# Kernel optimization log

Measured on AMD Instinct MI355X. Metric: run time of the kernel, lower is better.

Reference implementation:

```python
import jax, jax.numpy as jnp
import numpy as np

N_NODES = 50000
N_EDGES = 800000
IN_C, HID_C, OUT_C = 128, 128, 64
BN_EPS = 1e-5


def _normalized_adj(edge_index, N):
    # Mirrors remove_self_loops + add_self_loops + symmetric GCN normalization.
    src, dst = edge_index[0], edge_index[1]
    mask = (src != dst).astype(jnp.float32)  # drop original self loops
    # degree of dst over (masked edges + added self loops)
    deg = jax.ops.segment_sum(mask, dst, num_segments=N) + 1.0
    dinv = jnp.where(deg > 0, deg ** -0.5, 0.0)
    w = mask * dinv[src] * dinv[dst]          # weights for original edges
    w_self = dinv * dinv                      # weights for added self loops
    return src, dst, w, w_self


def _spmm(src, dst, w, w_self, x):
    # torch.sparse.mm(adj, x): out[i] = sum_{e: src[e]=i} w[e] * x[dst[e]] + w_self[i]*x[i]
    agg = jax.ops.segment_sum(w[:, None] * x[dst], src, num_segments=x.shape[0])
    return agg + w_self[:, None] * x


def setup_inputs() -> dict:
    key = jax.random.key(0)
    ks = jax.random.split(key, 4)
    x = jax.random.normal(ks[0], (N_NODES, IN_C), dtype=jnp.float32)
    edge_index = jax.random.randint(ks[1], (2, N_EDGES), 0, N_NODES, dtype=jnp.int64)
    # glorot init for GCN linear weights
    s1 = np.sqrt(6.0 / (IN_C + HID_C)).astype(np.float32)
    s2 = np.sqrt(6.0 / (HID_C + OUT_C)).astype(np.float32)
    W1 = jax.random.uniform(ks[2], (IN_C, HID_C), jnp.float32, -s1, s1)
    W2 = jax.random.uniform(ks[3], (HID_C, OUT_C), jnp.float32, -s2, s2)
    return {
        "x": x,
        "edge_index": edge_index,
        "W1": W1,
        "b1": jnp.zeros((HID_C,), jnp.float32),
        "gamma": jnp.ones((HID_C,), jnp.float32),
        "beta": jnp.zeros((HID_C,), jnp.float32),
        "W2": W2,
        "b2": jnp.zeros((OUT_C,), jnp.float32),
    }


def reference(x, edge_index, W1, b1, gamma, beta, W2, b2):
    N = x.shape[0]
    src, dst, w, w_self = _normalized_adj(edge_index, N)
    # layer 1: linear -> SpMM -> BN (batch stats) -> ReLU (dropout: eval)
    h = x @ W1 + b1
    h = _spmm(src, dst, w, w_self, h)
    mean = h.mean(axis=0)
    var = jnp.mean((h - mean) ** 2, axis=0)
    h = (h - mean) * jax.lax.rsqrt(var + BN_EPS) * gamma + beta
    h = jax.nn.relu(h)
    # layer 2: linear -> SpMM
    h = h @ W2 + b2
    h = _spmm(src, dst, w, w_self, h)
    return h
```

## Files before the change

### kernel.cpp

```cpp
#include <hip/hip_runtime.h>

#define N_NODES 50000
#define N_EDGES 800000
#define BN_EPS 1e-5f
#define NPAD 50176
#define SCAN_BLOCKS 98

#define S_SLICES 64
#define R_RANGES 7
#define BINS 8192
#define NP7 (R_RANGES * BINS)
#define ES (N_EDGES / S_SLICES)

#define XS_STRIDE 68

typedef unsigned int uint;
typedef unsigned short ushort;
typedef float floatx4 __attribute__((ext_vector_type(4)));
typedef short bf16x8 __attribute__((ext_vector_type(8)));

__device__ __forceinline__ float bfl(uint u) { return __uint_as_float(u << 16); }
__device__ __forceinline__ float bfh(uint u) { return __uint_as_float(u & 0xffff0000u); }
__device__ __forceinline__ uint pack_bf2(float a, float b) {
    uint ua = __float_as_uint(a), ub = __float_as_uint(b);
    ua += 0x7fffu + ((ua >> 16) & 1u);
    ub += 0x7fffu + ((ub >> 16) & 1u);
    return (ua >> 16) | (ub & 0xffff0000u);
}
__device__ __forceinline__ ushort bf1(float x) {
    uint u = __float_as_uint(x);
    u += 0x7fffu + ((u >> 16) & 1u);
    return (ushort)(u >> 16);
}
__device__ __forceinline__ void acc8(float* a, uint4 h, float w) {
    a[0] += w * bfl(h.x); a[1] += w * bfh(h.x);
    a[2] += w * bfl(h.y); a[3] += w * bfh(h.y);
    a[4] += w * bfl(h.z); a[5] += w * bfh(h.z);
    a[6] += w * bfl(h.w); a[7] += w * bfh(h.w);
}

__global__ __launch_bounds__(256) void prep_w_kernel(const float* __restrict__ W1,
                                                     const float* __restrict__ W2,
                                                     uint* __restrict__ W1t,
                                                     uint* __restrict__ W2t) {
    int t = blockIdx.x * 256 + threadIdx.x;
    if (t < 8192) {
        int n = t >> 6, kk = t & 63;
        W1t[t] = pack_bf2(W1[(2 * kk) * 128 + n], W1[(2 * kk + 1) * 128 + n]);
    } else if (t < 12288) {
        int u = t - 8192;
        int n = u >> 6, kk = u & 63;
        W2t[u] = pack_bf2(W2[(2 * kk) * 64 + n], W2[(2 * kk + 1) * 64 + n]);
    }
}

__global__ __launch_bounds__(256) void count_hist_kernel(const int* __restrict__ src,
                                                         const int* __restrict__ dst,
                                                         ushort* __restrict__ part_cnt,
                                                         ushort* __restrict__ part_deg) {
    __shared__ uint cnt_lds[BINS];
    __shared__ uint deg_lds[BINS];
    const int s = blockIdx.x / R_RANGES;
    const int r = blockIdx.x % R_RANGES;
    const int base = r * BINS;
    for (int j = threadIdx.x; j < BINS; j += 256) { cnt_lds[j] = 0u; deg_lds[j] = 0u; }
    __syncthreads();
    const int e0 = s * ES;
    for (int i = threadIdx.x; i < ES; i += 256) {
        int e = e0 + i;
        int ss = src[e], dd = dst[e];
        if (ss != dd) {
            int a = ss - base;
            if ((unsigned)a < (unsigned)BINS) atomicAdd(&cnt_lds[a], 1u);
            int b = dd - base;
            if ((unsigned)b < (unsigned)BINS) atomicAdd(&deg_lds[b], 1u);
        }
    }
    __syncthreads();
    uint* pc = (uint*)&part_cnt[s * NP7 + base];
    uint* pd = (uint*)&part_deg[s * NP7 + base];
    for (int j = threadIdx.x; j < BINS / 2; j += 256) {
        pc[j] = (cnt_lds[2 * j] & 0xffffu) | (cnt_lds[2 * j + 1] << 16);
        pd[j] = (deg_lds[2 * j] & 0xffffu) | (deg_lds[2 * j + 1] << 16);
    }
}

__global__ __launch_bounds__(256) void dinv_rowcnt_kernel(const ushort* __restrict__ part_deg,
                                                          const ushort* __restrict__ part_cnt,
                                                          float* __restrict__ dinv,
                                                          int* __restrict__ rowcnt) {
    int i = (blockIdx.x * 256 + threadIdx.x) * 2;
    uint dg0 = 0, dg1 = 0, rc0 = 0, rc1 = 0;
#pragma unroll 8
    for (int s = 0; s < S_SLICES; ++s) {
        uint vd = *(const uint*)&part_deg[s * NP7 + i];
        uint vc = *(const uint*)&part_cnt[s * NP7 + i];
        dg0 += vd & 0xffffu; dg1 += vd >> 16;
        rc0 += vc & 0xffffu; rc1 += vc >> 16;
    }
    *(int2*)&rowcnt[i] = make_int2((int)rc0, (int)rc1);
    if (i < N_NODES) dinv[i] = rsqrtf((float)dg0 + 1.0f);
    if (i + 1 < N_NODES) dinv[i + 1] = rsqrtf((float)dg1 + 1.0f);
}

__global__ __launch_bounds__(512) void scan1_kernel(const int* __restrict__ rowcnt,
                                                    int* __restrict__ rowptr,
                                                    int* __restrict__ psum) {
    __shared__ int buf[512];
    int t = threadIdx.x;
    int g = blockIdx.x * 512 + t;
    buf[t] = rowcnt[g];
    __syncthreads();
#pragma unroll
    for (int off = 1; off < 512; off <<= 1) {
        int x = (t >= off) ? buf[t - off] : 0;
        __syncthreads();
        buf[t] += x;
        __syncthreads();
    }
    rowptr[g] = buf[t];
    if (t == 511) psum[blockIdx.x] = buf[511];
}

__global__ void scan2_kernel(int* __restrict__ psum) {
    if (threadIdx.x == 0) {
        int acc = 0;
        for (int i = 0; i < SCAN_BLOCKS; ++i) {
            int v = psum[i];
            psum[i] = acc;
            acc += v;
        }
    }
}

__global__ __launch_bounds__(512) void scan3_kernel(const int* __restrict__ rowcnt,
                                                    int* __restrict__ rowptr,
                                                    const int* __restrict__ psum) {
    int t = threadIdx.x;
    int g = blockIdx.x * 512 + t;
    rowptr[g] = rowptr[g] - rowcnt[g] + psum[blockIdx.x];
}

__global__ __launch_bounds__(256) void cursor_init_kernel(const int* __restrict__ rowptr,
                                                          const ushort* __restrict__ part_cnt,
                                                          int* __restrict__ cursor) {
    int i = (blockIdx.x * 256 + threadIdx.x) * 2;
    int b0 = rowptr[i], b1 = rowptr[i + 1];
#pragma unroll 8
    for (int s = 0; s < S_SLICES; ++s) {
        *(int2*)&cursor[s * NP7 + i] = make_int2(b0, b1);
        uint vc = *(const uint*)&part_cnt[s * NP7 + i];
        b0 += (int)(vc & 0xffffu);
        b1 += (int)(vc >> 16);
    }
}

__global__ __launch_bounds__(256) void fill_lds_kernel(const int* __restrict__ src,
                                                       const int* __restrict__ dst,
                                                       const float* __restrict__ dinv,
                                                       const int* __restrict__ cursor,
                                                       int2* __restrict__ epair) {
    __shared__ int curs[BINS];
    const int s = blockIdx.x / R_RANGES;
    const int r = blockIdx.x % R_RANGES;
    const int base = r * BINS;
    const int* gc = &cursor[s * NP7 + base];
    for (int j = threadIdx.x; j < BINS; j += 256) curs[j] = gc[j];
    __syncthreads();
    const int e0 = s * ES;
    for (int i = threadIdx.x; i < ES; i += 256) {
        int e = e0 + i;
        int ss = src[e], dd = dst[e];
        int a = ss - base;
        if (ss != dd && (unsigned)a < (unsigned)BINS) {
            int pos = atomicAdd(&curs[a], 1);
            epair[pos] = make_int2(dd, __float_as_int(dinv[ss] * dinv[dd]));
        }
    }
}

__global__ __launch_bounds__(256) void gemm1_mfma_kernel(const float* __restrict__ X,
                                                         const uint* __restrict__ W1t,
                                                         const float* __restrict__ bias,
                                                         ushort* __restrict__ Hbf) {
    __shared__ uint lds[(64 + 128) * XS_STRIDE];
    uint* Xs = lds;
    uint* Ws = lds + 64 * XS_STRIDE;
    const int t = threadIdx.x;
    const int rowBase = blockIdx.x * 64;

    {
        int r = t >> 2, q = t & 3;
        int arow = rowBase + r;
        uint* xd = &Xs[r * XS_STRIDE + q * 16];
        if (arow < N_NODES) {
            const float4* xp = (const float4*)&X[arow * 128 + q * 32];
#pragma unroll
            for (int i = 0; i < 8; ++i) {
                float4 v = xp[i];
                xd[2 * i]     = pack_bf2(v.x, v.y);
                xd[2 * i + 1] = pack_bf2(v.z, v.w);
            }
        } else {
#pragma unroll
            for (int i = 0; i < 16; ++i) xd[i] = 0u;
        }
    }
    {
        int n = t >> 1, half = t & 1;
        const uint4* wp = (const uint4*)&W1t[n * 64 + half * 32];
        uint* wd = &Ws[n * XS_STRIDE + half * 32];
#pragma unroll
        for (int i = 0; i < 8; ++i) *(uint4*)&wd[i * 4] = wp[i];
    }
    __syncthreads();

    const int wv = t >> 6, lane = t & 63;
    const int lr = lane & 15;
    const int ko = (lane >> 4) * 4;
    const int m0 = wv * 16;
    floatx4 acc[8];
#pragma unroll
    for (int j = 0; j < 8; ++j) acc[j] = (floatx4){0.f, 0.f, 0.f, 0.f};

#pragma unroll
    for (int ks = 0; ks < 4; ++ks) {
        const int kb = ks * 16 + ko;
        bf16x8 a = *(bf16x8*)&Xs[(m0 + lr) * XS_STRIDE + kb];
#pragma unroll
        for (int j = 0; j < 8; ++j) {
            bf16x8 b = *(bf16x8*)&Ws[(j * 16 + lr) * XS_STRIDE + kb];
            acc[j] = __builtin_amdgcn_mfma_f32_16x16x32_bf16(a, b, acc[j], 0, 0, 0);
        }
    }
    const int rbase = rowBase + m0 + (lane >> 4) * 4;
#pragma unroll
    for (int j = 0; j < 8; ++j) {
        const int col = j * 16 + lr;
        const float bb = bias[col];
#pragma unroll
        for (int r = 0; r < 4; ++r) {
            int row = rbase + r;
            if (row < N_NODES) Hbf[row * 128 + col] = bf1(acc[j][r] + bb);
        }
    }
}

__global__ __launch_bounds__(256) void gemm2_mfma_kernel(const float* __restrict__ Hin,
                                                         const uint* __restrict__ W2t,
                                                         const float* __restrict__ bias,
                                                         const float* __restrict__ scale,
                                                         const float* __restrict__ shift,
                                                         ushort* __restrict__ Hbf) {
    __shared__ uint lds[(64 + 64) * XS_STRIDE];
    uint* Xs = lds;
    uint* Ws = lds + 64 * XS_STRIDE;
    const int t = threadIdx.x;
    const int rowBase = blockIdx.x * 64;

    {
        int r = t >> 2, q = t & 3;
        int arow = rowBase + r;
        uint* xd = &Xs[r * XS_STRIDE + q * 16];
        if (arow < N_NODES) {
            const float4* xp  = (const float4*)&Hin[arow * 128 + q * 32];
            const float4* sc4 = (const float4*)&scale[q * 32];
            const float4* sh4 = (const float4*)&shift[q * 32];
#pragma unroll
            for (int i = 0; i < 8; ++i) {
                float4 v = xp[i], sc = sc4[i], sh = sh4[i];
                float a0 = fmaxf(0.f, v.x * sc.x + sh.x);
                float a1 = fmaxf(0.f, v.y * sc.y + sh.y);
                float a2 = fmaxf(0.f, v.z * sc.z + sh.z);
                float a3 = fmaxf(0.f, v.w * sc.w + sh.w);
                xd[2 * i]     = pack_bf2(a0, a1);
                xd[2 * i + 1] = pack_bf2(a2, a3);
            }
        } else {
#pragma unroll
            for (int i = 0; i < 16; ++i) xd[i] = 0u;
        }
    }
    if (t < 128) {
        int n = t >> 1, half = t & 1;
        const uint4* wp = (const uint4*)&W2t[n * 64 + half * 32];
        uint* wd = &Ws[n * XS_STRIDE + half * 32];
#pragma unroll
        for (int i = 0; i < 8; ++i) *(uint4*)&wd[i * 4] = wp[i];
    }
    __syncthreads();

    const int wv = t >> 6, lane = t & 63;
    const int lr = lane & 15;
    const int ko = (lane >> 4) * 4;
    const int m0 = wv * 16;
    floatx4 acc[4];
#pragma unroll
    for (int j = 0; j < 4; ++j) acc[j] = (floatx4){0.f, 0.f, 0.f, 0.f};

#pragma unroll
    for (int ks = 0; ks < 4; ++ks) {
        const int kb = ks * 16 + ko;
        bf16x8 a = *(bf16x8*)&Xs[(m0 + lr) * XS_STRIDE + kb];
#pragma unroll
        for (int j = 0; j < 4; ++j) {
            bf16x8 b = *(bf16x8*)&Ws[(j * 16 + lr) * XS_STRIDE + kb];
            acc[j] = __builtin_amdgcn_mfma_f32_16x16x32_bf16(a, b, acc[j], 0, 0, 0);
        }
    }
    const int rbase = rowBase + m0 + (lane >> 4) * 4;
#pragma unroll
    for (int j = 0; j < 4; ++j) {
        const int col = j * 16 + lr;
        const float bb = bias[col];
#pragma unroll
        for (int r = 0; r < 4; ++r) {
            int row = rbase + r;
            if (row < N_NODES) Hbf[row * 64 + col] = bf1(acc[j][r] + bb);
        }
    }
}

template <int C>
__global__ __launch_bounds__(256) void spmm_bf16_kernel(const int* __restrict__ rowptr,
                                                        const int2* __restrict__ epair,
                                                        const float* __restrict__ dinv,
                                                        const uint* __restrict__ H,
                                                        float* __restrict__ out) {
    constexpr int LPR = C / 8;
    constexpr int RPB = 256 / LPR;
    constexpr int US  = C / 2;
    const int t = threadIdx.x;
    const int lane = t % LPR;
    const int row = blockIdx.x * RPB + t / LPR;
    if (row >= N_NODES) return;
    const int cu = lane * 4;
    const float di = dinv[row];

    float acc[8];
    {
        uint4 hv = *(const uint4*)&H[row * US + cu];
        float w = di * di;
        acc[0] = w * bfl(hv.x); acc[1] = w * bfh(hv.x);
        acc[2] = w * bfl(hv.y); acc[3] = w * bfh(hv.y);
        acc[4] = w * bfl(hv.z); acc[5] = w * bfh(hv.z);
        acc[6] = w * bfl(hv.w); acc[7] = w * bfh(hv.w);
    }
    const int e0 = rowptr[row], e1 = rowptr[row + 1];
    int e = e0;
    for (; e + 4 <= e1; e += 4) {
        int2 p0 = epair[e + 0], p1 = epair[e + 1], p2 = epair[e + 2], p3 = epair[e + 3];
        uint4 h0 = *(const uint4*)&H[p0.x * US + cu];
        uint4 h1 = *(const uint4*)&H[p1.x * US + cu];
        uint4 h2 = *(const uint4*)&H[p2.x * US + cu];
        uint4 h3 = *(const uint4*)&H[p3.x * US + cu];
        acc8(acc, h0, __int_as_float(p0.y));
        acc8(acc, h1, __int_as_float(p1.y));
        acc8(acc, h2, __int_as_float(p2.y));
        acc8(acc, h3, __int_as_float(p3.y));
    }
    for (; e < e1; ++e) {
        int2 p = epair[e];
        uint4 h = *(const uint4*)&H[p.x * US + cu];
        acc8(acc, h, __int_as_float(p.y));
    }
    float4 o0 = make_float4(acc[0], acc[1], acc[2], acc[3]);
    float4 o1 = make_float4(acc[4], acc[5], acc[6], acc[7]);
    *(float4*)&out[row * C + lane * 8] = o0;
    *(float4*)&out[row * C + lane * 8 + 4] = o1;
}

__global__ __launch_bounds__(256) void bn_stats_kernel(const float* __restrict__ H,
                                                       float* __restrict__ sum,
                                                       float* __restrict__ sumsq) {
    int c = threadIdx.x & 127;
    int half = threadIdx.x >> 7;
    float s = 0.f, q = 0.f;
    for (int r = blockIdx.x * 2 + half; r < N_NODES; r += 512) {
        float v = H[r * 128 + c];
        s += v;
        q += v * v;
    }
    __shared__ float ls[256], lq[256];
    ls[threadIdx.x] = s;
    lq[threadIdx.x] = q;
    __syncthreads();
    if (half == 0) {
        atomicAdd(&sum[c], ls[c] + ls[c + 128]);
        atomicAdd(&sumsq[c], lq[c] + lq[c + 128]);
    }
}

__global__ void bn_finalize_kernel(const float* __restrict__ sum,
                                   const float* __restrict__ sumsq,
                                   const float* __restrict__ gamma,
                                   const float* __restrict__ beta,
                                   float* __restrict__ scale,
                                   float* __restrict__ shift) {
    int c = threadIdx.x;
    if (c < 128) {
        float mean = sum[c] * (1.0f / N_NODES);
        float var = sumsq[c] * (1.0f / N_NODES) - mean * mean;
        float sc = gamma[c] * rsqrtf(var + BN_EPS);
        scale[c] = sc;
        shift[c] = beta[c] - mean * sc;
    }
}

extern "C" void kernel_launch(void* const* d_in, const int* in_sizes, int n_in,
                              void* d_out, int out_size, void* d_ws, size_t ws_size,
                              hipStream_t stream) {
    const float* x     = (const float*)d_in[0];
    const int*   ei    = (const int*)d_in[1];
    const float* W1    = (const float*)d_in[2];
    const float* b1    = (const float*)d_in[3];
    const float* gamma = (const float*)d_in[4];
    const float* beta  = (const float*)d_in[5];
    const float* W2    = (const float*)d_in[6];
    const float* b2    = (const float*)d_in[7];
    float* out = (float*)d_out;
    const int* src = ei;
    const int* dst = ei + N_EDGES;

    float* ws     = (float*)d_ws;
    float* dinv   = ws;
    float* stats  = ws + NPAD;
    int*   psum   = (int*)(ws + NPAD + 512);
    int*   rowcnt = psum + 128;
    int*   rowptr = rowcnt + NPAD;
    float* big    = (float*)(rowptr + NPAD);
    ushort* part_cnt = (ushort*)big;
    ushort* part_deg = part_cnt + S_SLICES * NP7;
    int*    cursor   = (int*)(part_deg + S_SLICES * NP7);
    ushort* h1bf  = (ushort*)big;
    float*  h1agg = big + 3200000;
    int2*   epair = (int2*)(big + 9600000);
    uint*   W1t   = (uint*)(big + 11200000);
    uint*   W2t   = W1t + 8192;
    ushort* h2bf  = h1bf;
    float* sum    = stats;
    float* sumsq  = stats + 128;
    float* scale  = stats + 256;
    float* shift  = stats + 384;

    hipMemsetAsync(stats, 0, 512 * sizeof(float), stream);

    prep_w_kernel<<<48, 256, 0, stream>>>(W1, W2, W1t, W2t);

    count_hist_kernel<<<S_SLICES * R_RANGES, 256, 0, stream>>>(src, dst, part_cnt, part_deg);
    dinv_rowcnt_kernel<<<NPAD / 512, 256, 0, stream>>>(part_deg, part_cnt, dinv, rowcnt);

    scan1_kernel<<<SCAN_BLOCKS, 512, 0, stream>>>(rowcnt, rowptr, psum);
    scan2_kernel<<<1, 64, 0, stream>>>(psum);
    scan3_kernel<<<SCAN_BLOCKS, 512, 0, stream>>>(rowcnt, rowptr, psum);
    cursor_init_kernel<<<NPAD / 512, 256, 0, stream>>>(rowptr, part_cnt, cursor);
    fill_lds_kernel<<<S_SLICES * R_RANGES, 256, 0, stream>>>(src, dst, dinv, cursor, epair);

    gemm1_mfma_kernel<<<(N_NODES + 63) / 64, 256, 0, stream>>>(x, W1t, b1, h1bf);

    spmm_bf16_kernel<128><<<(N_NODES + 15) / 16, 256, 0, stream>>>(rowptr, epair, dinv,
                                                                   (const uint*)h1bf, h1agg);

    bn_stats_kernel<<<256, 256, 0, stream>>>(h1agg, sum, sumsq);
    bn_finalize_kernel<<<1, 128, 0, stream>>>(sum, sumsq, gamma, beta, scale, shift);

    gemm2_mfma_kernel<<<(N_NODES + 63) / 64, 256, 0, stream>>>(h1agg, W2t, b2, scale, shift, h2bf);

    spmm_bf16_kernel<64><<<(N_NODES + 31) / 32, 256, 0, stream>>>(rowptr, epair, dinv,
                                                                  (const uint*)h2bf, out);
}
```

Measured before the change: 277.4 us.

## Store layer-1 SpMM output in bf16, degree-sort rows, pack 16-bit histograms, fuse scan

Several changes land together. The layer-1 SpMM now writes bf16 instead of fp32, which halves the traffic for bn_stats and gemm2, and bn_stats is rewritten to read packed bf16. Rows are permuted by degree bucket, built with a histogram, a scan and a scatter, so wavefronts in the SpMM kernels get similar loop lengths. The count histogram packs two 16-bit counters per LDS word, which allows 4 ranges of 16384 bins instead of 7 of 8192, and scan3 is folded into cursor_init. In exchange it adds three small kernels and bf16 rounding of pre-BN activations, and the permuted rows lose write locality.

```diff
diff --git a/kernel.cpp b/kernel.cpp
--- a/kernel.cpp
+++ b/kernel.cpp
@@ -7,9 +7,9 @@
 #define SCAN_BLOCKS 98
 
 #define S_SLICES 64
-#define R_RANGES 7
-#define BINS 8192
-#define NP7 (R_RANGES * BINS)
+#define R_RANGES 4
+#define BINS 16384
+#define NP4 (R_RANGES * BINS)
 #define ES (N_EDGES / S_SLICES)
 
 #define XS_STRIDE 68
@@ -58,12 +58,12 @@
                                                          const int* __restrict__ dst,
                                                          ushort* __restrict__ part_cnt,
                                                          ushort* __restrict__ part_deg) {
-    __shared__ uint cnt_lds[BINS];
-    __shared__ uint deg_lds[BINS];
+    __shared__ uint cnt_lds[BINS / 2];
+    __shared__ uint deg_lds[BINS / 2];
     const int s = blockIdx.x / R_RANGES;
     const int r = blockIdx.x % R_RANGES;
     const int base = r * BINS;
-    for (int j = threadIdx.x; j < BINS; j += 256) { cnt_lds[j] = 0u; deg_lds[j] = 0u; }
+    for (int j = threadIdx.x; j < BINS / 2; j += 256) { cnt_lds[j] = 0u; deg_lds[j] = 0u; }
     __syncthreads();
     const int e0 = s * ES;
     for (int i = threadIdx.x; i < ES; i += 256) {
@@ -71,18 +71,15 @@
         int ss = src[e], dd = dst[e];
         if (ss != dd) {
             int a = ss - base;
-            if ((unsigned)a < (unsigned)BINS) atomicAdd(&cnt_lds[a], 1u);
+            if ((unsigned)a < (unsigned)BINS) atomicAdd(&cnt_lds[a >> 1], 1u << ((a & 1) * 16));
             int b = dd - base;
-            if ((unsigned)b < (unsigned)BINS) atomicAdd(&deg_lds[b], 1u);
-        }
-    }
-    __syncthreads();
-    uint* pc = (uint*)&part_cnt[s * NP7 + base];
-    uint* pd = (uint*)&part_deg[s * NP7 + base];
-    for (int j = threadIdx.x; j < BINS / 2; j += 256) {
-        pc[j] = (cnt_lds[2 * j] & 0xffffu) | (cnt_lds[2 * j + 1] << 16);
-        pd[j] = (deg_lds[2 * j] & 0xffffu) | (deg_lds[2 * j + 1] << 16);
-    }
+            if ((unsigned)b < (unsigned)BINS) atomicAdd(&deg_lds[b >> 1], 1u << ((b & 1) * 16));
+        }
+    }
+    __syncthreads();
+    uint* pc = (uint*)&part_cnt[s * NP4 + base];
+    uint* pd = (uint*)&part_deg[s * NP4 + base];
+    for (int j = threadIdx.x; j < BINS / 2; j += 256) { pc[j] = cnt_lds[j]; pd[j] = deg_lds[j]; }
 }
 
 __global__ __launch_bounds__(256) void dinv_rowcnt_kernel(const ushort* __restrict__ part_deg,
@@ -93,8 +90,8 @@
     uint dg0 = 0, dg1 = 0, rc0 = 0, rc1 = 0;
 #pragma unroll 8
     for (int s = 0; s < S_SLICES; ++s) {
-        uint vd = *(const uint*)&part_deg[s * NP7 + i];
-        uint vc = *(const uint*)&part_cnt[s * NP7 + i];
+        uint vd = *(const uint*)&part_deg[s * NP4 + i];
+        uint vc = *(const uint*)&part_cnt[s * NP4 + i];
         dg0 += vd & 0xffffu; dg1 += vd >> 16;
         rc0 += vc & 0xffffu; rc1 += vc >> 16;
     }
@@ -133,23 +130,20 @@
     }
 }
 
-__global__ __launch_bounds__(512) void scan3_kernel(const int* __restrict__ rowcnt,
-                                                    int* __restrict__ rowptr,
-                                                    const int* __restrict__ psum) {
-    int t = threadIdx.x;
-    int g = blockIdx.x * 512 + t;
-    rowptr[g] = rowptr[g] - rowcnt[g] + psum[blockIdx.x];
-}
-
-__global__ __launch_bounds__(256) void cursor_init_kernel(const int* __restrict__ rowptr,
+__global__ __launch_bounds__(256) void cursor_init_kernel(const int* __restrict__ rowcnt,
+                                                          int* __restrict__ rowptr,
+                                                          const int* __restrict__ psum,
                                                           const ushort* __restrict__ part_cnt,
                                                           int* __restrict__ cursor) {
     int i = (blockIdx.x * 256 + threadIdx.x) * 2;
-    int b0 = rowptr[i], b1 = rowptr[i + 1];
+    int ps = psum[i >> 9];
+    int b0 = rowptr[i] - rowcnt[i] + ps;
+    int b1 = rowptr[i + 1] - rowcnt[i + 1] + ps;
+    *(int2*)&rowptr[i] = make_int2(b0, b1);
 #pragma unroll 8
     for (int s = 0; s < S_SLICES; ++s) {
-        *(int2*)&cursor[s * NP7 + i] = make_int2(b0, b1);
-        uint vc = *(const uint*)&part_cnt[s * NP7 + i];
+        *(int2*)&cursor[s * NP4 + i] = make_int2(b0, b1);
+        uint vc = *(const uint*)&part_cnt[s * NP4 + i];
         b0 += (int)(vc & 0xffffu);
         b1 += (int)(vc >> 16);
     }
@@ -164,7 +158,7 @@
     const int s = blockIdx.x / R_RANGES;
     const int r = blockIdx.x % R_RANGES;
     const int base = r * BINS;
-    const int* gc = &cursor[s * NP7 + base];
+    const int* gc = &cursor[s * NP4 + base];
     for (int j = threadIdx.x; j < BINS; j += 256) curs[j] = gc[j];
     __syncthreads();
     const int e0 = s * ES;
@@ -176,6 +170,38 @@
             int pos = atomicAdd(&curs[a], 1);
             epair[pos] = make_int2(dd, __float_as_int(dinv[ss] * dinv[dd]));
         }
+    }
+}
+
+__global__ __launch_bounds__(256) void deg_hist_kernel(const int* __restrict__ rowcnt,
+                                                       int* __restrict__ degh) {
+    int i = blockIdx.x * 256 + threadIdx.x;
+    if (i < N_NODES) atomicAdd(&degh[min(rowcnt[i], 1023)], 1);
+}
+
+__global__ __launch_bounds__(1024) void deg_scan_kernel(const int* __restrict__ degh,
+                                                        int* __restrict__ dcur) {
+    __shared__ int buf[1024];
+    int t = threadIdx.x;
+    buf[t] = degh[t];
+    __syncthreads();
+#pragma unroll
+    for (int off = 1; off < 1024; off <<= 1) {
+        int x = (t >= off) ? buf[t - off] : 0;
+        __syncthreads();
+        buf[t] += x;
+        __syncthreads();
+    }
+    dcur[t] = buf[t] - degh[t];
+}
+
+__global__ __launch_bounds__(256) void perm_scatter_kernel(const int* __restrict__ rowcnt,
+                                                           int* __restrict__ dcur,
+                                                           int* __restrict__ perm) {
+    int i = blockIdx.x * 256 + threadIdx.x;
+    if (i < N_NODES) {
+        int pos = atomicAdd(&dcur[min(rowcnt[i], 1023)], 1);
+        perm[pos] = i;
     }
 }
 
@@ -246,7 +272,7 @@
     }
 }
 
-__global__ __launch_bounds__(256) void gemm2_mfma_kernel(const float* __restrict__ Hin,
+__global__ __launch_bounds__(256) void gemm2_mfma_kernel(const uint* __restrict__ Hin,
                                                          const uint* __restrict__ W2t,
                                                          const float* __restrict__ bias,
                                                          const float* __restrict__ scale,
@@ -263,18 +289,16 @@
         int arow = rowBase + r;
         uint* xd = &Xs[r * XS_STRIDE + q * 16];
         if (arow < N_NODES) {
-            const float4* xp  = (const float4*)&Hin[arow * 128 + q * 32];
-            const float4* sc4 = (const float4*)&scale[q * 32];
-            const float4* sh4 = (const float4*)&shift[q * 32];
-#pragma unroll
-            for (int i = 0; i < 8; ++i) {
-                float4 v = xp[i], sc = sc4[i], sh = sh4[i];
-                float a0 = fmaxf(0.f, v.x * sc.x + sh.x);
-                float a1 = fmaxf(0.f, v.y * sc.y + sh.y);
-                float a2 = fmaxf(0.f, v.z * sc.z + sh.z);
-                float a3 = fmaxf(0.f, v.w * sc.w + sh.w);
-                xd[2 * i]     = pack_bf2(a0, a1);
-                xd[2 * i + 1] = pack_bf2(a2, a3);
+            const uint* hp = &Hin[arow * 64 + q * 16];
+#pragma unroll
+            for (int i = 0; i < 16; ++i) {
+                uint u = hp[i];
+                int m = q * 16 + i;
+                float2 sc = *(const float2*)&scale[2 * m];
+                float2 sh = *(const float2*)&shift[2 * m];
+                float a0 = fmaxf(0.f, bfl(u) * sc.x + sh.x);
+                float a1 = fmaxf(0.f, bfh(u) * sc.y + sh.y);
+                xd[i] = pack_bf2(a0, a1);
             }
         } else {
 #pragma unroll
@@ -321,19 +345,21 @@
     }
 }
 
-template <int C>
+template <int C, bool OUT_BF16>
 __global__ __launch_bounds__(256) void spmm_bf16_kernel(const int* __restrict__ rowptr,
                                                         const int2* __restrict__ epair,
                                                         const float* __restrict__ dinv,
+                                                        const int* __restrict__ perm,
                                                         const uint* __restrict__ H,
-                                                        float* __restrict__ out) {
+                                                        void* __restrict__ outv) {
     constexpr int LPR = C / 8;
     constexpr int RPB = 256 / LPR;
     constexpr int US  = C / 2;
     const int t = threadIdx.x;
     const int lane = t % LPR;
-    const int row = blockIdx.x * RPB + t / LPR;
-    if (row >= N_NODES) return;
+    const int g = blockIdx.x * RPB + t / LPR;
+    if (g >= N_NODES) return;
+    const int row = perm[g];
     const int cu = lane * 4;
     const float di = dinv[row];
 
@@ -364,30 +390,47 @@
         uint4 h = *(const uint4*)&H[p.x * US + cu];
         acc8(acc, h, __int_as_float(p.y));
     }
-    float4 o0 = make_float4(acc[0], acc[1], acc[2], acc[3]);
-    float4 o1 = make_float4(acc[4], acc[5], acc[6], acc[7]);
-    *(float4*)&out[row * C + lane * 8] = o0;
-    *(float4*)&out[row * C + lane * 8 + 4] = o1;
-}
-
-__global__ __launch_bounds__(256) void bn_stats_kernel(const float* __restrict__ H,
+    if (OUT_BF16) {
+        uint4 o;
+        o.x = pack_bf2(acc[0], acc[1]);
+        o.y = pack_bf2(acc[2], acc[3]);
+        o.z = pack_bf2(acc[4], acc[5]);
+        o.w = pack_bf2(acc[6], acc[7]);
+        *(uint4*)&((uint*)outv)[row * US + cu] = o;
+    } else {
+        float* out = (float*)outv;
+        *(float4*)&out[row * C + lane * 8]     = make_float4(acc[0], acc[1], acc[2], acc[3]);
+        *(float4*)&out[row * C + lane * 8 + 4] = make_float4(acc[4], acc[5], acc[6], acc[7]);
+    }
+}
+
+__global__ __launch_bounds__(256) void bn_stats_kernel(const uint* __restrict__ H,
                                                        float* __restrict__ sum,
                                                        float* __restrict__ sumsq) {
-    int c = threadIdx.x & 127;
-    int half = threadIdx.x >> 7;
-    float s = 0.f, q = 0.f;
-    for (int r = blockIdx.x * 2 + half; r < N_NODES; r += 512) {
-        float v = H[r * 128 + c];
-        s += v;
-        q += v * v;
-    }
-    __shared__ float ls[256], lq[256];
-    ls[threadIdx.x] = s;
-    lq[threadIdx.x] = q;
-    __syncthreads();
-    if (half == 0) {
-        atomicAdd(&sum[c], ls[c] + ls[c + 128]);
-        atomicAdd(&sumsq[c], lq[c] + lq[c + 128]);
+    int uc = threadIdx.x & 63;
+    int quarter = threadIdx.x >> 6;
+    float s0 = 0.f, q0 = 0.f, s1 = 0.f, q1 = 0.f;
+    for (int r = blockIdx.x * 4 + quarter; r < N_NODES; r += 512) {
+        uint u = H[r * 64 + uc];
+        float a = bfl(u), b = bfh(u);
+        s0 += a; q0 += a * a;
+        s1 += b; q1 += b * b;
+    }
+    __shared__ float red[4][256];
+    red[0][threadIdx.x] = s0; red[1][threadIdx.x] = q0;
+    red[2][threadIdx.x] = s1; red[3][threadIdx.x] = q1;
+    __syncthreads();
+    if (quarter == 0) {
+        float ts0 = 0.f, tq0 = 0.f, ts1 = 0.f, tq1 = 0.f;
+#pragma unroll
+        for (int k = 0; k < 4; ++k) {
+            ts0 += red[0][k * 64 + uc]; tq0 += red[1][k * 64 + uc];
+            ts1 += red[2][k * 64 + uc]; tq1 += red[3][k * 64 + uc];
+        }
+        atomicAdd(&sum[2 * uc], ts0);
+        atomicAdd(&sum[2 * uc + 1], ts1);
+        atomicAdd(&sumsq[2 * uc], tq0);
+        atomicAdd(&sumsq[2 * uc + 1], tq1);
     }
 }
 
@@ -425,25 +468,28 @@
     float* ws     = (float*)d_ws;
     float* dinv   = ws;
     float* stats  = ws + NPAD;
-    int*   psum   = (int*)(ws + NPAD + 512);
+    int*   degh   = (int*)(ws + NPAD + 512);
+    int*   dcur   = degh + 1024;
+    int*   psum   = dcur + 1024;
     int*   rowcnt = psum + 128;
     int*   rowptr = rowcnt + NPAD;
-    float* big    = (float*)(rowptr + NPAD);
-    ushort* part_cnt = (ushort*)big;
-    ushort* part_deg = part_cnt + S_SLICES * NP7;
-    int*    cursor   = (int*)(part_deg + S_SLICES * NP7);
-    ushort* h1bf  = (ushort*)big;
-    float*  h1agg = big + 3200000;
-    int2*   epair = (int2*)(big + 9600000);
-    uint*   W1t   = (uint*)(big + 11200000);
-    uint*   W2t   = W1t + 8192;
-    ushort* h2bf  = h1bf;
+    int*   perm   = rowptr + NPAD;
+    float* big    = (float*)(perm + NPAD);
+    int2*   epair    = (int2*)big;
+    ushort* part_cnt = (ushort*)(big + 1600000);
+    ushort* part_deg = (ushort*)(big + 3700000);
+    int*    cursor   = (int*)(big + 5800000);
+    ushort* h1bf     = (ushort*)(big + 1600000);
+    uint*   h1agg    = (uint*)(big + 4800000);
+    ushort* h2bf     = h1bf;
+    uint*   W1t      = (uint*)(big + 10000000);
+    uint*   W2t      = W1t + 8192;
     float* sum    = stats;
     float* sumsq  = stats + 128;
     float* scale  = stats + 256;
     float* shift  = stats + 384;
 
-    hipMemsetAsync(stats, 0, 512 * sizeof(float), stream);
+    hipMemsetAsync(stats, 0, (512 + 1024) * sizeof(float), stream);
 
     prep_w_kernel<<<48, 256, 0, stream>>>(W1, W2, W1t, W2t);
 
@@ -452,20 +498,23 @@
 
     scan1_kernel<<<SCAN_BLOCKS, 512, 0, stream>>>(rowcnt, rowptr, psum);
     scan2_kernel<<<1, 64, 0, stream>>>(psum);
-    scan3_kernel<<<SCAN_BLOCKS, 512, 0, stream>>>(rowcnt, rowptr, psum);
-    cursor_init_kernel<<<NPAD / 512, 256, 0, stream>>>(rowptr, part_cnt, cursor);
+    cursor_init_kernel<<<NPAD / 512, 256, 0, stream>>>(rowcnt, rowptr, psum, part_cnt, cursor);
     fill_lds_kernel<<<S_SLICES * R_RANGES, 256, 0, stream>>>(src, dst, dinv, cursor, epair);
 
+    deg_hist_kernel<<<(N_NODES + 255) / 256, 256, 0, stream>>>(rowcnt, degh);
+    deg_scan_kernel<<<1, 1024, 0, stream>>>(degh, dcur);
+    perm_scatter_kernel<<<(N_NODES + 255) / 256, 256, 0, stream>>>(rowcnt, dcur, perm);
+
     gemm1_mfma_kernel<<<(N_NODES + 63) / 64, 256, 0, stream>>>(x, W1t, b1, h1bf);
 
-    spmm_bf16_kernel<128><<<(N_NODES + 15) / 16, 256, 0, stream>>>(rowptr, epair, dinv,
-                                                                   (const uint*)h1bf, h1agg);
-
-    bn_stats_kernel<<<256, 256, 0, stream>>>(h1agg, sum, sumsq);
+    spmm_bf16_kernel<128, true><<<(N_NODES + 15) / 16, 256, 0, stream>>>(
+        rowptr, epair, dinv, perm, (const uint*)h1bf, (void*)h1agg);
+
+    bn_stats_kernel<<<128, 256, 0, stream>>>(h1agg, sum, sumsq);
     bn_finalize_kernel<<<1, 128, 0, stream>>>(sum, sumsq, gamma, beta, scale, shift);
 
     gemm2_mfma_kernel<<<(N_NODES + 63) / 64, 256, 0, stream>>>(h1agg, W2t, b2, scale, shift, h2bf);
 
-    spmm_bf16_kernel<64><<<(N_NODES + 31) / 32, 256, 0, stream>>>(rowptr, epair, dinv,
-                                                                  (const uint*)h2bf, out);
-}
+    spmm_bf16_kernel<64, false><<<(N_NODES + 31) / 32, 256, 0, stream>>>(
+        rowptr, epair, dinv, perm, (const uint*)h2bf, (void*)out);
+}
```

Result: slower. 538.5 us (+94.1%).
